# Kernel tuning notes

Measured on AMD Instinct MI355X. Metric: run time of the kernel, lower is better.

The kernel has to match this reference:

```python
import jax, jax.numpy as jnp
import numpy as np

E, K, H, I = 64, 8, 2048, 768  # num_experts, top_k, hidden, moe_intermediate

def setup_inputs() -> dict:
    key = jax.random.key(0)
    k1, k2, k3, k4 = jax.random.split(key, 4)
    return {
        "hidden_states": jax.random.normal(k1, (1, 1024, H), dtype=jnp.float32),
        "w_gate": jax.random.normal(k2, (H, E), dtype=jnp.float32) * 0.02,
        "w13": jax.random.normal(k3, (E, H, 2 * I), dtype=jnp.float32) * 0.02,  # fused gate+up proj
        "w2": jax.random.normal(k4, (E, I, H), dtype=jnp.float32) * 0.02,
    }

def reference(hidden_states, w_gate, w13, w2):
    orig_shape = hidden_states.shape
    x = hidden_states.reshape(-1, orig_shape[-1])            # [T, H]
    T = x.shape[0]

    # Router: logits -> softmax -> top-k -> renormalize (norm_topk_prob=True)
    router_logits = x @ w_gate                               # [T, E]
    probs = jax.nn.softmax(router_logits, axis=-1)
    topk_w, topk_idx = jax.lax.top_k(probs, K)               # [T, K]
    topk_w = topk_w / jnp.sum(topk_w, axis=-1, keepdims=True)
    # Dense combine-weight matrix [T, E] (zero for non-routed experts)
    combine = jnp.zeros((T, E), dtype=x.dtype).at[
        jnp.arange(T)[:, None], topk_idx].add(topk_w)

    # Expert SwiGLU FFN, computed densely for all experts, masked by combine
    h = jnp.einsum('th,ehd->etd', x, w13)                    # [E, T, 2I]
    gate, up = h[..., :I], h[..., I:]
    act = jax.nn.silu(gate) * up                             # [E, T, I]
    y = jnp.einsum('eti,eih->eth', act, w2)                  # [E, T, H]
    out = jnp.einsum('eth,te->th', y, combine)               # [T, H]
    return out.reshape(orig_shape)
```

## Files before the change

### kernel.cpp

```cpp
#include <hip/hip_runtime.h>
#include <hip/hip_bf16.h>
#include <math.h>

#define NE 64
#define NK 8
#define NH 2048
#define NI 768
#define NT 1024
#define BP 40
#define BSUB (128 * BP)

typedef float f32x4 __attribute__((ext_vector_type(4)));
typedef __bf16 bf16x8 __attribute__((ext_vector_type(8)));
typedef __bf16 bf16x4 __attribute__((ext_vector_type(4)));

__global__ __launch_bounds__(256) void router_k(
    const float* __restrict__ x, const float* __restrict__ wg,
    __bf16* __restrict__ x_bf, int* __restrict__ topk_idx,
    float* __restrict__ topk_w)
{
    __shared__ float xs[4][NH];
    const int wave = threadIdx.x >> 6;
    const int lane = threadIdx.x & 63;
    const int t = blockIdx.x * 4 + wave;

    const float* xrow = x + (size_t)t * NH;
    __bf16* brow = x_bf + (size_t)t * NH;
    #pragma unroll
    for (int j = 0; j < 8; ++j) {
        int idx = j * 256 + lane * 4;
        f32x4 v = *reinterpret_cast<const f32x4*>(xrow + idx);
        *reinterpret_cast<f32x4*>(&xs[wave][idx]) = v;
        bf16x4 b;
        b[0] = (__bf16)v.x; b[1] = (__bf16)v.y; b[2] = (__bf16)v.z; b[3] = (__bf16)v.w;
        *reinterpret_cast<bf16x4*>(brow + idx) = b;
    }
    __syncthreads();

    float a0 = 0.f, a1 = 0.f, a2 = 0.f, a3 = 0.f;
    for (int h = 0; h < NH; h += 4) {
        a0 = fmaf(xs[wave][h + 0], wg[(h + 0) * NE + lane], a0);
        a1 = fmaf(xs[wave][h + 1], wg[(h + 1) * NE + lane], a1);
        a2 = fmaf(xs[wave][h + 2], wg[(h + 2) * NE + lane], a2);
        a3 = fmaf(xs[wave][h + 3], wg[(h + 3) * NE + lane], a3);
    }
    float acc = (a0 + a1) + (a2 + a3);

    float cur = acc;
    float sel_v[NK]; int sel_i[NK];
    #pragma unroll
    for (int k = 0; k < NK; ++k) {
        float bv = cur; int bi = lane;
        #pragma unroll
        for (int s = 32; s; s >>= 1) {
            float ov = __shfl_xor(bv, s, 64);
            int   oi = __shfl_xor(bi, s, 64);
            if (ov > bv || (ov == bv && oi < bi)) { bv = ov; bi = oi; }
        }
        sel_v[k] = bv; sel_i[k] = bi;
        if (lane == bi) cur = -3.4e38f;
    }
    float m = sel_v[0];
    float ssum = 0.f;
    #pragma unroll
    for (int k = 0; k < NK; ++k) ssum += expf(sel_v[k] - m);

    if (lane < NK) {
        float w = expf(sel_v[lane] - m) / ssum;
        topk_idx[t * NK + lane] = sel_i[lane];
        topk_w[t * NK + lane] = w;
    }
}

__global__ __launch_bounds__(256) void scanscatter_k(
    const int* __restrict__ topk_idx, const float* __restrict__ topk_w,
    int* __restrict__ counts, int* __restrict__ offs,
    int* __restrict__ slot_tok, float* __restrict__ slot_w,
    int* __restrict__ slot_of)
{
    __shared__ int hist[NE], base[NE], cur[NE];
    const int tid = threadIdx.x;
    if (tid < NE) hist[tid] = 0;
    __syncthreads();
    for (int i = tid; i < NT * NK; i += 256)
        atomicAdd(&hist[topk_idx[i]], 1);
    __syncthreads();
    if (tid == 0) {
        int r = 0;
        for (int e = 0; e < NE; ++e) { base[e] = r; r += hist[e]; }
    }
    __syncthreads();
    if (tid < NE) { counts[tid] = hist[tid]; offs[tid] = base[tid]; cur[tid] = 0; }
    __syncthreads();
    for (int i = tid; i < NT * NK; i += 256) {
        int e = topk_idx[i];
        int p = atomicAdd(&cur[e], 1);
        int g = base[e] + p;
        slot_tok[g] = i >> 3;
        slot_w[g] = topk_w[i];
        slot_of[i] = g;
    }
}

__global__ __launch_bounds__(256, 2) void e1_k(
    const __bf16* __restrict__ x_bf, const float* __restrict__ w13,
    const int* __restrict__ counts, const int* __restrict__ offs,
    const int* __restrict__ slot_tok, __bf16* __restrict__ act)
{
    const int e = blockIdx.x;
    const int cnt = counts[e];
    const int m0 = blockIdx.z * 256;
    if (m0 >= cnt) return;
    const int rows = min(256, cnt - m0);
    const int n0 = blockIdx.y * 64;
    const int goff = offs[e] + m0;

    __shared__ __bf16 B[2][2 * BSUB];
    __shared__ int tok[256];

    const int tid = threadIdx.x;
    tok[tid] = (tid < rows) ? slot_tok[goff + tid] : slot_tok[goff];
    __syncthreads();

    const int wave = tid >> 6, lane = tid & 63;
    f32x4 acc[4][8];
    #pragma unroll
    for (int i = 0; i < 4; ++i)
        #pragma unroll
        for (int j = 0; j < 8; ++j) acc[i][j] = (f32x4){0.f, 0.f, 0.f, 0.f};

    const __bf16* ap[4];
    bool mok[4];
    #pragma unroll
    for (int mf = 0; mf < 4; ++mf) {
        int rf = mf * 64 + wave * 16;
        mok[mf] = (rf < rows);
        int arow = rf + (lane & 15);
        ap[mf] = x_bf + (size_t)tok[arow] * NH + ((lane >> 4) << 3);
    }

    const float* w13e = w13 + (size_t)e * NH * (2 * NI);
    const int cc = tid & 31, kch = tid >> 5;
    const int bcol0 = cc * 4;
    const int gcol = (bcol0 < 64) ? (n0 + bcol0) : (NI + n0 + bcol0 - 64);
    const int rot = (cc >> 1) & 3;
    const float* bptr = w13e + (size_t)(kch * 4) * (2 * NI) + gcol;
    int bj[4], boff[4];
    #pragma unroll
    for (int jj = 0; jj < 4; ++jj) {
        int j = (jj + rot) & 3;
        bj[jj] = j;
        boff[jj] = (bcol0 + j) * BP + kch * 4;
    }

    f32x4 bReg[2][4];
    auto loadT = [&](int kk) {
        #pragma unroll
        for (int s = 0; s < 2; ++s)
            #pragma unroll
            for (int ki = 0; ki < 4; ++ki)
                bReg[s][ki] = *reinterpret_cast<const f32x4*>(
                    bptr + (size_t)(kk + s * 32 + ki) * (2 * NI));
    };
    auto writeT = [&](int buf) {
        #pragma unroll
        for (int s = 0; s < 2; ++s)
            #pragma unroll
            for (int jj = 0; jj < 4; ++jj) {
                int j = bj[jj];
                bf16x4 p;
                p[0] = (__bf16)bReg[s][0][j]; p[1] = (__bf16)bReg[s][1][j];
                p[2] = (__bf16)bReg[s][2][j]; p[3] = (__bf16)bReg[s][3][j];
                *reinterpret_cast<bf16x4*>(&B[buf][s * BSUB + boff[jj]]) = p;
            }
    };
    auto compute = [&](int buf) {
        #pragma unroll
        for (int kk = 0; kk < 2; ++kk) {
            bf16x8 av[4];
            #pragma unroll
            for (int mf = 0; mf < 4; ++mf)
                if (mok[mf]) av[mf] = *reinterpret_cast<const bf16x8*>(ap[mf] + kk * 32);
            bf16x8 bfr[8];
            #pragma unroll
            for (int nf = 0; nf < 8; ++nf) {
                int col = nf * 16 + (lane & 15);
                bfr[nf] = *reinterpret_cast<const bf16x8*>(
                    &B[buf][kk * BSUB + col * BP + ((lane >> 4) << 3)]);
            }
            #pragma unroll
            for (int mf = 0; mf < 4; ++mf)
                if (mok[mf])
                    #pragma unroll
                    for (int nf = 0; nf < 8; ++nf)
                        acc[mf][nf] = __builtin_amdgcn_mfma_f32_16x16x32_bf16(
                            av[mf], bfr[nf], acc[mf][nf], 0, 0, 0);
        }
        #pragma unroll
        for (int mf = 0; mf < 4; ++mf) ap[mf] += 64;
    };

    loadT(0);
    writeT(0);
    __syncthreads();

    #pragma unroll 1
    for (int t = 0; t < 32; ++t) {
        if (t + 1 < 32) loadT((t + 1) * 64);
        compute(t & 1);
        if (t + 1 < 32) writeT((t + 1) & 1);
        __syncthreads();
    }

    #pragma unroll
    for (int mf = 0; mf < 4; ++mf) {
        int rf = mf * 64 + wave * 16;
        if (rf >= rows) continue;
        #pragma unroll
        for (int nf = 0; nf < 4; ++nf) {
            f32x4 g = acc[mf][nf];
            f32x4 u = acc[mf][nf + 4];
            int col = n0 + nf * 16 + (lane & 15);
            #pragma unroll
            for (int r = 0; r < 4; ++r) {
                int row = rf + ((lane >> 4) << 2) + r;
                if (row < rows) {
                    float gv = g[r];
                    float a = gv / (1.f + expf(-gv)) * u[r];
                    act[(size_t)(goff + row) * NI + col] = (__bf16)a;
                }
            }
        }
    }
}

__global__ __launch_bounds__(256, 2) void e2_k(
    const __bf16* __restrict__ act, const float* __restrict__ w2,
    const int* __restrict__ counts, const int* __restrict__ offs,
    const float* __restrict__ slot_w, __bf16* __restrict__ partial)
{
    const int e = blockIdx.x;
    const int cnt = counts[e];
    const int m0 = blockIdx.z * 256;
    if (m0 >= cnt) return;
    const int rows = min(256, cnt - m0);
    const int n0 = blockIdx.y * 128;
    const int goff = offs[e] + m0;

    __shared__ __bf16 B[2][2 * BSUB];

    const int tid = threadIdx.x, wave = tid >> 6, lane = tid & 63;
    f32x4 acc[4][8];
    #pragma unroll
    for (int i = 0; i < 4; ++i)
        #pragma unroll
        for (int j = 0; j < 8; ++j) acc[i][j] = (f32x4){0.f, 0.f, 0.f, 0.f};

    const __bf16* ap[4];
    bool mok[4];
    #pragma unroll
    for (int mf = 0; mf < 4; ++mf) {
        int rf = mf * 64 + wave * 16;
        mok[mf] = (rf < rows);
        int arow = goff + rf + (lane & 15);
        ap[mf] = act + (size_t)arow * NI + ((lane >> 4) << 3);
    }

    const float* w2e = w2 + (size_t)e * NI * NH;
    const int cc = tid & 31, kch = tid >> 5;
    const int bcol0 = cc * 4;
    const int rot = (cc >> 1) & 3;
    const float* bptr = w2e + (size_t)(kch * 4) * NH + n0 + bcol0;
    int bj[4], boff[4];
    #pragma unroll
    for (int jj = 0; jj < 4; ++jj) {
        int j = (jj + rot) & 3;
        bj[jj] = j;
        boff[jj] = (bcol0 + j) * BP + kch * 4;
    }

    f32x4 bReg[2][4];
    auto loadT = [&](int kk) {
        #pragma unroll
        for (int s = 0; s < 2; ++s)
            #pragma unroll
            for (int ki = 0; ki < 4; ++ki)
                bReg[s][ki] = *reinterpret_cast<const f32x4*>(
                    bptr + (size_t)(kk + s * 32 + ki) * NH);
    };
    auto writeT = [&](int buf) {
        #pragma unroll
        for (int s = 0; s < 2; ++s)
            #pragma unroll
            for (int jj = 0; jj < 4; ++jj) {
                int j = bj[jj];
                bf16x4 p;
                p[0] = (__bf16)bReg[s][0][j]; p[1] = (__bf16)bReg[s][1][j];
                p[2] = (__bf16)bReg[s][2][j]; p[3] = (__bf16)bReg[s][3][j];
                *reinterpret_cast<bf16x4*>(&B[buf][s * BSUB + boff[jj]]) = p;
            }
    };
    auto compute = [&](int buf) {
        #pragma unroll
        for (int kk = 0; kk < 2; ++kk) {
            bf16x8 av[4];
            #pragma unroll
            for (int mf = 0; mf < 4; ++mf)
                if (mok[mf]) av[mf] = *reinterpret_cast<const bf16x8*>(ap[mf] + kk * 32);
            bf16x8 bfr[8];
            #pragma unroll
            for (int nf = 0; nf < 8; ++nf) {
                int col = nf * 16 + (lane & 15);
                bfr[nf] = *reinterpret_cast<const bf16x8*>(
                    &B[buf][kk * BSUB + col * BP + ((lane >> 4) << 3)]);
            }
            #pragma unroll
            for (int mf = 0; mf < 4; ++mf)
                if (mok[mf])
                    #pragma unroll
                    for (int nf = 0; nf < 8; ++nf)
                        acc[mf][nf] = __builtin_amdgcn_mfma_f32_16x16x32_bf16(
                            av[mf], bfr[nf], acc[mf][nf], 0, 0, 0);
        }
        #pragma unroll
        for (int mf = 0; mf < 4; ++mf) ap[mf] += 64;
    };

    loadT(0);
    writeT(0);
    __syncthreads();

    #pragma unroll 1
    for (int t = 0; t < 12; ++t) {
        if (t + 1 < 12) loadT((t + 1) * 64);
        compute(t & 1);
        if (t + 1 < 12) writeT((t + 1) & 1);
        __syncthreads();
    }

    #pragma unroll
    for (int mf = 0; mf < 4; ++mf) {
        int rf = mf * 64 + wave * 16;
        if (rf >= rows) continue;
        int rb = rf + ((lane >> 4) << 2);
        #pragma unroll
        for (int r = 0; r < 4; ++r) {
            int row = rb + r;
            if (row >= rows) continue;
            int gs = goff + row;
            float wv = slot_w[gs];
            #pragma unroll
            for (int nf = 0; nf < 8; ++nf) {
                int col = n0 + nf * 16 + (lane & 15);
                partial[(size_t)gs * NH + col] = (__bf16)(wv * acc[mf][nf][r]);
            }
        }
    }
}

__global__ __launch_bounds__(256) void combine_k(
    const __bf16* __restrict__ partial, const int* __restrict__ slot_of,
    float* __restrict__ out)
{
    const int t = blockIdx.x;
    const int c0 = threadIdx.x * 8;
    __shared__ int gs[NK];
    if (threadIdx.x < NK) gs[threadIdx.x] = slot_of[t * NK + threadIdx.x];
    __syncthreads();

    float s[8] = {0.f, 0.f, 0.f, 0.f, 0.f, 0.f, 0.f, 0.f};
    #pragma unroll
    for (int k = 0; k < NK; ++k) {
        bf16x8 v = *reinterpret_cast<const bf16x8*>(partial + (size_t)gs[k] * NH + c0);
        #pragma unroll
        for (int j = 0; j < 8; ++j) s[j] += (float)v[j];
    }
    f32x4 o0 = {s[0], s[1], s[2], s[3]};
    f32x4 o1 = {s[4], s[5], s[6], s[7]};
    *reinterpret_cast<f32x4*>(out + (size_t)t * NH + c0) = o0;
    *reinterpret_cast<f32x4*>(out + (size_t)t * NH + c0 + 4) = o1;
}

extern "C" void kernel_launch(void* const* d_in, const int* in_sizes, int n_in,
                              void* d_out, int out_size, void* d_ws, size_t ws_size,
                              hipStream_t stream)
{
    const float* x   = (const float*)d_in[0];
    const float* wg  = (const float*)d_in[1];
    const float* w13 = (const float*)d_in[2];
    const float* w2  = (const float*)d_in[3];
    float* out = (float*)d_out;
    char* ws = (char*)d_ws;

    __bf16* x_bf = (__bf16*)ws;
    size_t o = (size_t)4 * 1024 * 1024;
    __bf16* act = (__bf16*)(ws + o);      o += (size_t)8192 * NI * 2;
    __bf16* partial = (__bf16*)(ws + o);  o += (size_t)8192 * NH * 2;
    int*   topk_idx = (int*)(ws + o);     o += 8192 * 4;
    float* topk_w   = (float*)(ws + o);   o += 8192 * 4;
    int*   slot_tok = (int*)(ws + o);     o += 8192 * 4;
    float* slot_w   = (float*)(ws + o);   o += 8192 * 4;
    int*   slot_of  = (int*)(ws + o);     o += 8192 * 4;
    int*   counts   = (int*)(ws + o);     o += 256;
    int*   offs     = (int*)(ws + o);     o += 256;

    router_k    <<<NT / 4, 256, 0, stream>>>(x, wg, x_bf, topk_idx, topk_w);
    scanscatter_k<<<1, 256, 0, stream>>>(topk_idx, topk_w, counts, offs,
                                         slot_tok, slot_w, slot_of);
    e1_k<<<dim3(NE, NI / 64, 2), 256, 0, stream>>>(x_bf, w13, counts, offs, slot_tok, act);
    e2_k<<<dim3(NE, NH / 128, 2), 256, 0, stream>>>(act, w2, counts, offs, slot_w, partial);
    combine_k<<<NT, 256, 0, stream>>>(partial, slot_of, out);
}
```

Before: 441.7 us.

## Narrow e1 tile to 32 columns, use nontemporal weight loads, widen scatter block

The e1 kernel now covers 32 gate/up columns per block instead of 64. That doubles the grid, halves accumulator and LDS use, and raises the occupancy hint to 3 blocks per SM. Weight loads in e1 and e2 use nontemporal loads so the streamed fp32 weights do not pollute the cache. The single-block scan/scatter kernel runs with 1024 threads instead of 256. The narrower tile re-reads each gathered activation row twice as often and lowers MFMA work per LDS load, trading that reuse for more parallelism and latency hiding.

```diff
diff --git a/kernel.cpp b/kernel.cpp
--- a/kernel.cpp
+++ b/kernel.cpp
@@ -8,7 +8,8 @@
 #define NI 768
 #define NT 1024
 #define BP 40
-#define BSUB (128 * BP)
+#define SUB64 (64 * BP)
+#define SUB128 (128 * BP)
 
 typedef float f32x4 __attribute__((ext_vector_type(4)));
 typedef __bf16 bf16x8 __attribute__((ext_vector_type(8)));
@@ -72,7 +73,7 @@
     }
 }
 
-__global__ __launch_bounds__(256) void scanscatter_k(
+__global__ __launch_bounds__(1024) void scanscatter_k(
     const int* __restrict__ topk_idx, const float* __restrict__ topk_w,
     int* __restrict__ counts, int* __restrict__ offs,
     int* __restrict__ slot_tok, float* __restrict__ slot_w,
@@ -82,7 +83,7 @@
     const int tid = threadIdx.x;
     if (tid < NE) hist[tid] = 0;
     __syncthreads();
-    for (int i = tid; i < NT * NK; i += 256)
+    for (int i = tid; i < NT * NK; i += 1024)
         atomicAdd(&hist[topk_idx[i]], 1);
     __syncthreads();
     if (tid == 0) {
@@ -92,7 +93,7 @@
     __syncthreads();
     if (tid < NE) { counts[tid] = hist[tid]; offs[tid] = base[tid]; cur[tid] = 0; }
     __syncthreads();
-    for (int i = tid; i < NT * NK; i += 256) {
+    for (int i = tid; i < NT * NK; i += 1024) {
         int e = topk_idx[i];
         int p = atomicAdd(&cur[e], 1);
         int g = base[e] + p;
@@ -102,7 +103,7 @@
     }
 }
 
-__global__ __launch_bounds__(256, 2) void e1_k(
+__global__ __launch_bounds__(256, 3) void e1_k(
     const __bf16* __restrict__ x_bf, const float* __restrict__ w13,
     const int* __restrict__ counts, const int* __restrict__ offs,
     const int* __restrict__ slot_tok, __bf16* __restrict__ act)
@@ -112,10 +113,10 @@
     const int m0 = blockIdx.z * 256;
     if (m0 >= cnt) return;
     const int rows = min(256, cnt - m0);
-    const int n0 = blockIdx.y * 64;
+    const int n0 = blockIdx.y * 32;
     const int goff = offs[e] + m0;
 
-    __shared__ __bf16 B[2][2 * BSUB];
+    __shared__ __bf16 B[2][2 * SUB64];
     __shared__ int tok[256];
 
     const int tid = threadIdx.x;
@@ -123,11 +124,11 @@
     __syncthreads();
 
     const int wave = tid >> 6, lane = tid & 63;
-    f32x4 acc[4][8];
+    f32x4 acc[4][4];
     #pragma unroll
     for (int i = 0; i < 4; ++i)
         #pragma unroll
-        for (int j = 0; j < 8; ++j) acc[i][j] = (f32x4){0.f, 0.f, 0.f, 0.f};
+        for (int j = 0; j < 4; ++j) acc[i][j] = (f32x4){0.f, 0.f, 0.f, 0.f};
 
     const __bf16* ap[4];
     bool mok[4];
@@ -140,39 +141,36 @@
     }
 
     const float* w13e = w13 + (size_t)e * NH * (2 * NI);
-    const int cc = tid & 31, kch = tid >> 5;
+    const int cc = tid & 15, kch = tid >> 4;
     const int bcol0 = cc * 4;
-    const int gcol = (bcol0 < 64) ? (n0 + bcol0) : (NI + n0 + bcol0 - 64);
+    const int gcol = (bcol0 < 32) ? (n0 + bcol0) : (NI + n0 + bcol0 - 32);
     const int rot = (cc >> 1) & 3;
     const float* bptr = w13e + (size_t)(kch * 4) * (2 * NI) + gcol;
+    const int sub = kch >> 3, kloc = kch & 7;
     int bj[4], boff[4];
     #pragma unroll
     for (int jj = 0; jj < 4; ++jj) {
         int j = (jj + rot) & 3;
         bj[jj] = j;
-        boff[jj] = (bcol0 + j) * BP + kch * 4;
-    }
-
-    f32x4 bReg[2][4];
+        boff[jj] = sub * SUB64 + (bcol0 + j) * BP + kloc * 4;
+    }
+
+    f32x4 bReg[4];
     auto loadT = [&](int kk) {
         #pragma unroll
-        for (int s = 0; s < 2; ++s)
-            #pragma unroll
-            for (int ki = 0; ki < 4; ++ki)
-                bReg[s][ki] = *reinterpret_cast<const f32x4*>(
-                    bptr + (size_t)(kk + s * 32 + ki) * (2 * NI));
+        for (int ki = 0; ki < 4; ++ki)
+            bReg[ki] = __builtin_nontemporal_load(
+                reinterpret_cast<const f32x4*>(bptr + (size_t)(kk + ki) * (2 * NI)));
     };
     auto writeT = [&](int buf) {
         #pragma unroll
-        for (int s = 0; s < 2; ++s)
-            #pragma unroll
-            for (int jj = 0; jj < 4; ++jj) {
-                int j = bj[jj];
-                bf16x4 p;
-                p[0] = (__bf16)bReg[s][0][j]; p[1] = (__bf16)bReg[s][1][j];
-                p[2] = (__bf16)bReg[s][2][j]; p[3] = (__bf16)bReg[s][3][j];
-                *reinterpret_cast<bf16x4*>(&B[buf][s * BSUB + boff[jj]]) = p;
-            }
+        for (int jj = 0; jj < 4; ++jj) {
+            int j = bj[jj];
+            bf16x4 p;
+            p[0] = (__bf16)bReg[0][j]; p[1] = (__bf16)bReg[1][j];
+            p[2] = (__bf16)bReg[2][j]; p[3] = (__bf16)bReg[3][j];
+            *reinterpret_cast<bf16x4*>(&B[buf][boff[jj]]) = p;
+        }
     };
     auto compute = [&](int buf) {
         #pragma unroll
@@ -181,18 +179,18 @@
             #pragma unroll
             for (int mf = 0; mf < 4; ++mf)
                 if (mok[mf]) av[mf] = *reinterpret_cast<const bf16x8*>(ap[mf] + kk * 32);
-            bf16x8 bfr[8];
-            #pragma unroll
-            for (int nf = 0; nf < 8; ++nf) {
+            bf16x8 bfr[4];
+            #pragma unroll
+            for (int nf = 0; nf < 4; ++nf) {
                 int col = nf * 16 + (lane & 15);
                 bfr[nf] = *reinterpret_cast<const bf16x8*>(
-                    &B[buf][kk * BSUB + col * BP + ((lane >> 4) << 3)]);
+                    &B[buf][kk * SUB64 + col * BP + ((lane >> 4) << 3)]);
             }
             #pragma unroll
             for (int mf = 0; mf < 4; ++mf)
                 if (mok[mf])
                     #pragma unroll
-                    for (int nf = 0; nf < 8; ++nf)
+                    for (int nf = 0; nf < 4; ++nf)
                         acc[mf][nf] = __builtin_amdgcn_mfma_f32_16x16x32_bf16(
                             av[mf], bfr[nf], acc[mf][nf], 0, 0, 0);
         }
@@ -217,9 +215,9 @@
         int rf = mf * 64 + wave * 16;
         if (rf >= rows) continue;
         #pragma unroll
-        for (int nf = 0; nf < 4; ++nf) {
+        for (int nf = 0; nf < 2; ++nf) {
             f32x4 g = acc[mf][nf];
-            f32x4 u = acc[mf][nf + 4];
+            f32x4 u = acc[mf][nf + 2];
             int col = n0 + nf * 16 + (lane & 15);
             #pragma unroll
             for (int r = 0; r < 4; ++r) {
@@ -247,7 +245,7 @@
     const int n0 = blockIdx.y * 128;
     const int goff = offs[e] + m0;
 
-    __shared__ __bf16 B[2][2 * BSUB];
+    __shared__ __bf16 B[2][2 * SUB128];
 
     const int tid = threadIdx.x, wave = tid >> 6, lane = tid & 63;
     f32x4 acc[4][8];
@@ -285,8 +283,8 @@
         for (int s = 0; s < 2; ++s)
             #pragma unroll
             for (int ki = 0; ki < 4; ++ki)
-                bReg[s][ki] = *reinterpret_cast<const f32x4*>(
-                    bptr + (size_t)(kk + s * 32 + ki) * NH);
+                bReg[s][ki] = __builtin_nontemporal_load(
+                    reinterpret_cast<const f32x4*>(bptr + (size_t)(kk + s * 32 + ki) * NH));
     };
     auto writeT = [&](int buf) {
         #pragma unroll
@@ -297,7 +295,7 @@
                 bf16x4 p;
                 p[0] = (__bf16)bReg[s][0][j]; p[1] = (__bf16)bReg[s][1][j];
                 p[2] = (__bf16)bReg[s][2][j]; p[3] = (__bf16)bReg[s][3][j];
-                *reinterpret_cast<bf16x4*>(&B[buf][s * BSUB + boff[jj]]) = p;
+                *reinterpret_cast<bf16x4*>(&B[buf][s * SUB128 + boff[jj]]) = p;
             }
     };
     auto compute = [&](int buf) {
@@ -312,7 +310,7 @@
             for (int nf = 0; nf < 8; ++nf) {
                 int col = nf * 16 + (lane & 15);
                 bfr[nf] = *reinterpret_cast<const bf16x8*>(
-                    &B[buf][kk * BSUB + col * BP + ((lane >> 4) << 3)]);
+                    &B[buf][kk * SUB128 + col * BP + ((lane >> 4) << 3)]);
             }
             #pragma unroll
             for (int mf = 0; mf < 4; ++mf)
@@ -405,9 +403,9 @@
     int*   offs     = (int*)(ws + o);     o += 256;
 
     router_k    <<<NT / 4, 256, 0, stream>>>(x, wg, x_bf, topk_idx, topk_w);
-    scanscatter_k<<<1, 256, 0, stream>>>(topk_idx, topk_w, counts, offs,
-                                         slot_tok, slot_w, slot_of);
-    e1_k<<<dim3(NE, NI / 64, 2), 256, 0, stream>>>(x_bf, w13, counts, offs, slot_tok, act);
+    scanscatter_k<<<1, 1024, 0, stream>>>(topk_idx, topk_w, counts, offs,
+                                          slot_tok, slot_w, slot_of);
+    e1_k<<<dim3(NE, NI / 32, 2), 256, 0, stream>>>(x_bf, w13, counts, offs, slot_tok, act);
     e2_k<<<dim3(NE, NH / 128, 2), 256, 0, stream>>>(act, w2, counts, offs, slot_w, partial);
     combine_k<<<NT, 256, 0, stream>>>(partial, slot_of, out);
 }
```

New measurement: 396.6 us. 10.2% less time.
